# Kernel optimization log

Hardware: AMD Instinct MI355X
Metric: run time of the kernel (lower is better)

## Reference

```python
import jax, jax.numpy as jnp
import numpy as np

N = 50000   # nodes of ntype 'A'
E = 800000  # edges per metapath
M = 4       # metapaths (first-order, tail = 'A')
H = 4       # attn heads
C = 32      # out_channels = output_dim // attn_heads
IN = 256    # input_dim
D = H * C   # output_dim = 128
NEG_SLOPE = 0.2


def setup_inputs() -> dict:
    key = jax.random.key(0)
    ks = jax.random.split(key, 8)
    feats = jax.random.normal(ks[0], (N, IN), dtype=jnp.float32)
    edge_index = jax.random.randint(ks[1], (M, 2, E), 0, N, dtype=jnp.int32)
    W = jax.random.normal(ks[2], (IN, D), dtype=jnp.float32) * (2.0 / (IN + D)) ** 0.5
    b = jnp.zeros((D,), dtype=jnp.float32)
    attn = jax.random.normal(ks[3], (M, H, 2 * C), dtype=jnp.float32) * 0.1
    rel_attn_l = jax.random.normal(ks[4], (H, C), dtype=jnp.float32) * 0.1
    rel_attn_r = jax.random.normal(ks[5], (M + 1, H, C), dtype=jnp.float32) * 0.1
    rel_attn_bias = jnp.zeros((M + 1,), dtype=jnp.float32)
    return {"feats": feats, "edge_index": edge_index, "W": W, "b": b,
            "attn": attn, "rel_attn_l": rel_attn_l, "rel_attn_r": rel_attn_r,
            "rel_attn_bias": rel_attn_bias}


def _segment_softmax(logits, seg, num_segments):
    # logits: [E, H], seg: [E] target-node ids; softmax over incoming edges per node.
    seg_max = jax.ops.segment_max(logits, seg, num_segments=num_segments)  # [N, H]
    e = jnp.exp(logits - seg_max[seg])
    seg_sum = jax.ops.segment_sum(e, seg, num_segments=num_segments)       # [N, H]
    return e / (seg_sum[seg] + 1e-16)


def reference(feats, edge_index, W, b, attn, rel_attn_l, rel_attn_r, rel_attn_bias):
    # projection: per-ntype Linear + relu, reshape to heads
    h = jax.nn.relu(feats @ W + b).reshape(N, H, C)  # l_dict == r_dict == h

    # per-metapath GAT-style propagate (aggr='add')
    rels = []
    for m in range(M):
        src = edge_index[m, 0]
        dst = edge_index[m, 1]
        x_j = h[src]  # [E, H, C] source messages
        x_i = h[dst]  # [E, H, C] target queries
        # alpha = (cat([x_i, x_j], -1) * attn[m]).sum(-1), LeakyReLU(0.2)
        logits = jnp.einsum('ehc,hc->eh', x_i, attn[m, :, :C]) \
               + jnp.einsum('ehc,hc->eh', x_j, attn[m, :, C:])
        logits = jax.nn.leaky_relu(logits, NEG_SLOPE)
        alpha = _segment_softmax(logits, dst, N)                 # [E, H]
        out = jax.ops.segment_sum(x_j * alpha[..., None], dst, num_segments=N)  # [N, H, C]
        rels.append(out)
    rels.append(h)  # last relation slot = self (embedding[:, -1] = l_dict[ntype])
    emb = jnp.stack(rels, axis=1)  # [N, M+1, H, C]

    # beta relation-attention weights
    beta_l = jax.nn.relu(h * rel_attn_l)                          # [N, H, C]
    beta_r = jax.nn.relu(emb * rel_attn_r)                        # [N, M+1, H, C]
    beta = jnp.einsum('nhc,nrhc->nrh', beta_l, beta_r) + rel_attn_bias[None, :, None]
    beta = jax.nn.softmax(beta, axis=1)                           # over relations

    emb = (emb * beta[..., None]).sum(axis=1).reshape(N, D)
    return jax.nn.relu(emb)
```

## Files before the change

kernel.cpp:

```cpp
#include <hip/hip_runtime.h>
#include <math.h>

#define kN 50000
#define kE 800000
#define kM 4
#define kH 4
#define kC 32
#define kIN 256
#define kD 128

typedef __attribute__((ext_vector_type(8))) short bf16x8;
typedef __attribute__((ext_vector_type(4))) float f32x4;

__device__ __forceinline__ unsigned int f2bf_pack(float a, float b) {
    unsigned ua = __float_as_uint(a);
    ua += 0x7fffu + ((ua >> 16) & 1u);
    unsigned ub = __float_as_uint(b);
    ub += 0x7fffu + ((ub >> 16) & 1u);
    return (ua >> 16) | (ub & 0xffff0000u);
}
__device__ __forceinline__ unsigned short f2bf(float x) {
    unsigned u = __float_as_uint(x);
    u += 0x7fffu + ((u >> 16) & 1u);
    return (unsigned short)(u >> 16);
}

#define NBK 98
#define BCAP 10240
#define MW (NBK * BCAP)
#define PAB ((kE + 4095) / 4096)

__global__ void k_wcast(const float* __restrict__ W, unsigned short* __restrict__ Wt16) {
    const int col = blockIdx.x;
    const int k = threadIdx.x;
    Wt16[(size_t)col * kIN + k] = f2bf(W[(size_t)k * kD + col]);
}

#define GEMMB ((kN + 127) / 128)
__global__ __launch_bounds__(256) void k_gemmbucket(const float* __restrict__ feats,
                                                    const unsigned short* __restrict__ Wt16,
                                                    const float* __restrict__ b,
                                                    const float* __restrict__ attn,
                                                    unsigned short* __restrict__ h16,
                                                    float* __restrict__ sl,
                                                    float* __restrict__ sr,
                                                    const int* __restrict__ ei,
                                                    int* __restrict__ bcur,
                                                    unsigned int* __restrict__ pairs) {
    __shared__ __align__(16) unsigned char smem[64 * 130 * 2];
    __shared__ int hist[NBK], h2[NBK], base_s[NBK];
    const int t = threadIdx.x;

    if (blockIdx.x >= GEMMB) {
        const int bi = blockIdx.x - GEMMB;
        const int m = bi / PAB;
        const int chunk = bi - m * PAB;
        const int e0 = chunk * 4096;
        for (int j = t; j < NBK; j += 256) { hist[j] = 0; h2[j] = 0; }
        __syncthreads();
        int src[16], dst[16];
#pragma unroll
        for (int i = 0; i < 16; i++) {
            const int e = e0 + i * 256 + t;
            const int eok = (e < kE) ? e : 0;
            src[i] = ei[(size_t)m * 2 * kE + eok];
            dst[i] = (e < kE) ? ei[(size_t)m * 2 * kE + kE + eok] : -1;
        }
#pragma unroll
        for (int i = 0; i < 16; i++)
            if (dst[i] >= 0) atomicAdd(&hist[dst[i] >> 9], 1);
        __syncthreads();
        for (int j = t; j < NBK; j += 256)
            base_s[j] = atomicAdd(&bcur[m * NBK + j], hist[j]);
        __syncthreads();
#pragma unroll
        for (int i = 0; i < 16; i++) {
            if (dst[i] >= 0) {
                const int bk = dst[i] >> 9;
                const int slot = base_s[bk] + atomicAdd(&h2[bk], 1);
                pairs[(size_t)m * MW + (size_t)bk * BCAP + slot] =
                    ((unsigned int)(dst[i] & 511) << 16) | (unsigned int)src[i];
            }
        }
        return;
    }

    unsigned short* fr16 = reinterpret_cast<unsigned short*>(smem);
    typedef unsigned short hrow_t[130];
    hrow_t* hlds = reinterpret_cast<hrow_t*>(smem);

    const int lane = t & 63;
    const int wave = t >> 6;
    const int q = lane >> 4;
    const int m16 = lane & 15;
    const int wrow = (wave >> 1) * 64;
    const int wcol = (wave & 1) * 64;
    const int rowbase = blockIdx.x * 128;

    f32x4 acc[4][4];
#pragma unroll
    for (int i = 0; i < 4; i++)
#pragma unroll
        for (int j = 0; j < 4; j++) acc[i][j] = (f32x4){0.f, 0.f, 0.f, 0.f};

    const int srow = t >> 3;
    const int sk4 = t & 7;

    for (int kc = 0; kc < kIN; kc += 32) {
        __syncthreads();
#pragma unroll
        for (int it = 0; it < 4; it++) {
            const int row = srow + it * 32;
            const int rg = rowbase + row;
            float4 v = make_float4(0.f, 0.f, 0.f, 0.f);
            if (rg < kN)
                v = *reinterpret_cast<const float4*>(feats + (size_t)rg * kIN + kc + sk4 * 4);
            uint2 p;
            p.x = f2bf_pack(v.x, v.y);
            p.y = f2bf_pack(v.z, v.w);
            *reinterpret_cast<uint2*>(&fr16[row * 32 + sk4 * 4]) = p;
        }
        __syncthreads();

        bf16x8 afr[4], bfr[4];
#pragma unroll
        for (int ri = 0; ri < 4; ri++)
            afr[ri] = *reinterpret_cast<const bf16x8*>(
                &fr16[(wrow + ri * 16 + m16) * 32 + q * 8]);
#pragma unroll
        for (int ci = 0; ci < 4; ci++)
            bfr[ci] = *reinterpret_cast<const bf16x8*>(
                Wt16 + (size_t)(wcol + ci * 16 + m16) * kIN + kc + q * 8);
#pragma unroll
        for (int ri = 0; ri < 4; ri++)
#pragma unroll
            for (int ci = 0; ci < 4; ci++)
                acc[ri][ci] = __builtin_amdgcn_mfma_f32_16x16x32_bf16(
                    afr[ri], bfr[ci], acc[ri][ci], 0, 0, 0);
    }

    float bcol[4];
#pragma unroll
    for (int ci = 0; ci < 4; ci++) bcol[ci] = b[wcol + ci * 16 + m16];

#pragma unroll
    for (int ri = 0; ri < 4; ri++) {
#pragma unroll
        for (int reg = 0; reg < 4; reg++) {
            const int row = wrow + ri * 16 + q * 4 + reg;
            const int rg = rowbase + row;
            if (rg < kN) {
#pragma unroll
                for (int ci = 0; ci < 4; ci++) {
                    const int col = wcol + ci * 16 + m16;
                    const float v = fmaxf(acc[ri][ci][reg] + bcol[ci], 0.f);
                    h16[(size_t)rg * kD + col] = f2bf(v);
                }
            }
        }
    }
    __syncthreads();

    const unsigned int* hl32 = reinterpret_cast<const unsigned int*>(smem);
#pragma unroll
    for (int half = 0; half < 2; half++) {
        if ((wrow >> 6) == half) {
#pragma unroll
            for (int ri = 0; ri < 4; ri++)
#pragma unroll
                for (int reg = 0; reg < 4; reg++) {
                    const int row = (wrow & 63) + ri * 16 + q * 4 + reg;
#pragma unroll
                    for (int ci = 0; ci < 4; ci++) {
                        const int col = wcol + ci * 16 + m16;
                        const float v = fmaxf(acc[ri][ci][reg] + bcol[ci], 0.f);
                        hlds[row][col] = f2bf(v);
                    }
                }
        }
        __syncthreads();
        {
            const int hh = t & 3;
            const int nl = t >> 2;
            const int n = rowbase + half * 64 + nl;
            if (n < kN) {
                unsigned int u[16];
#pragma unroll
                for (int k = 0; k < 16; k++) u[k] = hl32[nl * 65 + hh * 16 + k];
                float f0[16], f1[16];
#pragma unroll
                for (int k = 0; k < 16; k++) {
                    f0[k] = __uint_as_float(u[k] << 16);
                    f1[k] = __uint_as_float(u[k] & 0xffff0000u);
                }
#pragma unroll
                for (int m = 0; m < kM; m++) {
                    const float2* al = reinterpret_cast<const float2*>(attn + (m * kH + hh) * 2 * kC);
                    const float2* ar = al + 16;
                    float s0 = 0.f, s1 = 0.f;
#pragma unroll
                    for (int k = 0; k < 16; k++) {
                        const float2 a = al[k], r = ar[k];
                        s0 += f0[k] * a.x + f1[k] * a.y;
                        s1 += f0[k] * r.x + f1[k] * r.y;
                    }
                    sl[((size_t)m * kN + n) * kH + hh] = s0;
                    sr[((size_t)m * kN + n) * kH + hh] = s1;
                }
            }
        }
        __syncthreads();
    }
}

#define SORTB (kM * NBK)
__global__ __launch_bounds__(256) void k_sort(const unsigned int* __restrict__ pairs,
                                              const int* __restrict__ bcur,
                                              int* __restrict__ offs,
                                              int* __restrict__ cnta,
                                              unsigned short* __restrict__ srcsort) {
    __shared__ int hist[512], pref[512], h2[512], wt[4];
    const int t = threadIdx.x;
    const int m = blockIdx.x / NBK;
    const int bk = blockIdx.x - m * NBK;
    const int bs = bk << 9;
    const int base = bk * BCAP;
    const int n = bcur[m * NBK + bk];
    const unsigned int* __restrict__ pb = pairs + (size_t)m * MW + base;
    unsigned short* __restrict__ ss = srcsort + (size_t)m * MW + base;

    hist[t] = 0; hist[t + 256] = 0; h2[t] = 0; h2[t + 256] = 0;
    __syncthreads();

    unsigned int v[40];
#pragma unroll
    for (int j = 0; j < 40; j++) {
        const int idx = j * 256 + t;
        v[j] = (idx < n) ? pb[idx] : 0xffffffffu;
    }
#pragma unroll
    for (int j = 0; j < 40; j++)
        if (v[j] != 0xffffffffu) atomicAdd(&hist[v[j] >> 16], 1);
    __syncthreads();

    const int lane = t & 63, wid = t >> 6;
    const int j0 = 2 * t, j1 = 2 * t + 1;
    const int h0 = hist[j0], h1 = hist[j1];
    const int s = h0 + h1;
    int incl = s;
#pragma unroll
    for (int d = 1; d < 64; d <<= 1) {
        const int x = __shfl_up(incl, d);
        if (lane >= d) incl += x;
    }
    if (lane == 63) wt[wid] = incl;
    __syncthreads();
    int woff = 0;
#pragma unroll
    for (int i = 0; i < 4; i++)
        if (i < wid) woff += wt[i];
    const int excl = woff + incl - s;
    pref[j0] = excl;
    pref[j1] = excl + h0;
    const int d0 = bs + j0, d1 = bs + j1;
    if (d0 < kN) { offs[m * kN + d0] = base + excl;       cnta[m * kN + d0] = h0; }
    if (d1 < kN) { offs[m * kN + d1] = base + excl + h0;  cnta[m * kN + d1] = h1; }
    __syncthreads();

#pragma unroll
    for (int j = 0; j < 40; j++) {
        if (v[j] != 0xffffffffu) {
            const int dl = (int)(v[j] >> 16);
            const int pos = pref[dl] + atomicAdd(&h2[dl], 1);
            ss[pos] = (unsigned short)(v[j] & 0xffffu);
        }
    }
    if (t < 64 && n + t < BCAP) ss[n + t] = 0;
}

#define CH 16

#define AGG_BODY(GN)                                                            \
    {                                                                           \
        int sj[GN];                                                             \
        _Pragma("unroll")                                                       \
        for (int j = 0; j < GN; j++) {                                          \
            const int id = __builtin_amdgcn_readlane(my0, j);                   \
            sj[j] = (j < nb) ? id : dst;                                        \
        }                                                                       \
        unsigned int u[GN];                                                     \
        _Pragma("unroll")                                                       \
        for (int j = 0; j < GN; j++)                                            \
            u[j] = *reinterpret_cast<const unsigned int*>(                      \
                hb + (((size_t)(unsigned int)sj[j] << 8) + ebyte));             \
        float x = sl_h + srv;                                                   \
        x = x > 0.f ? x : 0.2f * x;                         \
        const float w = (c + jj < cnt) ? __expf(x) : 0.f;                       \
        sum += w;                                                               \
        swts[m][l] = w;                                                         \
        __builtin_amdgcn_wave_barrier();                                        \
        const float4 w0 = *reinterpret_cast<const float4*>(&swts[m][hh * 16]);  \
        const float4 w1 = *reinterpret_cast<const float4*>(&swts[m][hh*16+4]);  \
        const float4 w2 = *reinterpret_cast<const float4*>(&swts[m][hh*16+8]);  \
        const float4 w3 = *reinterpret_cast<const float4*>(&swts[m][hh*16+12]); \
        __builtin_amdgcn_wave_barrier();                                        \
        my0 = my1;                                                              \
        my1 = sbase[c + 2 * CH + jj];                                           \
        srv = *reinterpret_cast<const float*>(                                  \
            srb + (((unsigned int)my0 << 4) + hbyte));                          \
        const float wj[16] = {w0.x, w0.y, w0.z, w0.w, w1.x, w1.y, w1.z, w1.w,   \
                              w2.x, w2.y, w2.z, w2.w, w3.x, w3.y, w3.z, w3.w};  \
        _Pragma("unroll")                                                       \
        for (int j = 0; j < GN; j++) {                                          \
            a0 += wj[j] * __uint_as_float(u[j] << 16);                          \
            a1 += wj[j] * __uint_as_float(u[j] & 0xffff0000u);                  \
        }                                                                       \
    }

__global__ __launch_bounds__(256) void k_agg(const unsigned short* __restrict__ h16,
                                             const float* __restrict__ sl,
                                             const float* __restrict__ sr,
                                             const int* __restrict__ offs,
                                             const int* __restrict__ cnta,
                                             const unsigned short* __restrict__ srcsort,
                                             const float* __restrict__ ral,
                                             const float* __restrict__ rar,
                                             const float* __restrict__ rbias,
                                             float* __restrict__ out) {
    const int dst = blockIdx.x;
    const int t = threadIdx.x;
    const int m = t >> 6;
    const int l = t & 63;
    const int hh = l >> 4;
    const int jj = l & 15;
    const int e0 = l * 2;

    __shared__ float smres[kM][kD];
    __shared__ float swts[kM][64];

    const int beg = offs[m * kN + dst];
    const int cnt = cnta[m * kN + dst];
    const float sl_h = sl[((size_t)m * kN + dst) * kH + hh];
    const unsigned short* __restrict__ sbase = srcsort + (size_t)m * MW + beg;
    const char* __restrict__ hb = (const char*)h16;
    const char* __restrict__ srb = (const char*)(sr + (size_t)m * kN * kH);
    const unsigned int ebyte = (unsigned int)(e0 << 1);
    const unsigned int hbyte = (unsigned int)(hh << 2);

    float sum = 0.f, a0 = 0.f, a1 = 0.f;

    int my0 = sbase[jj];
    int my1 = sbase[CH + jj];
    float srv = *reinterpret_cast<const float*>(
        srb + (((unsigned int)my0 << 4) + hbyte));

    for (int c = 0; c < cnt; c += CH) {
        const int nb = cnt - c;
        if (nb >= 9) AGG_BODY(16) else AGG_BODY(8)
    }

    sum += __shfl_xor(sum, 1);
    sum += __shfl_xor(sum, 2);
    sum += __shfl_xor(sum, 4);
    sum += __shfl_xor(sum, 8);
    const float inv = 1.0f / (sum + 1e-16f);
    smres[m][e0] = a0 * inv;
    smres[m][e0 + 1] = a1 * inv;
    __syncthreads();

    if (m == 0) {
        const unsigned int ud = *reinterpret_cast<const unsigned int*>(
            hb + (((unsigned int)dst << 8) + ebyte));
        const float hd0 = __uint_as_float(ud << 16);
        const float hd1 = __uint_as_float(ud & 0xffff0000u);
        const float bl0 = fmaxf(hd0 * ral[e0], 0.f);
        const float bl1 = fmaxf(hd1 * ral[e0 + 1], 0.f);
        float emb0[5], emb1[5], beta[5];
#pragma unroll
        for (int r = 0; r < 5; r++) {
            const float x0 = (r < 4) ? smres[r][e0] : hd0;
            const float x1 = (r < 4) ? smres[r][e0 + 1] : hd1;
            emb0[r] = x0;
            emb1[r] = x1;
            const float br0 = fmaxf(x0 * rar[r * kD + e0], 0.f);
            const float br1 = fmaxf(x1 * rar[r * kD + e0 + 1], 0.f);
            float p = bl0 * br0 + bl1 * br1;
            p += __shfl_xor(p, 1);
            p += __shfl_xor(p, 2);
            p += __shfl_xor(p, 4);
            p += __shfl_xor(p, 8);
            beta[r] = p + rbias[r];
        }
        float mx = beta[0];
#pragma unroll
        for (int r = 1; r < 5; r++) mx = fmaxf(mx, beta[r]);
        float s = 0.f, wgt[5];
#pragma unroll
        for (int r = 0; r < 5; r++) { wgt[r] = __expf(beta[r] - mx); s += wgt[r]; }
        const float invb = 1.f / s;
        float o0 = 0.f, o1 = 0.f;
#pragma unroll
        for (int r = 0; r < 5; r++) { o0 += emb0[r] * wgt[r]; o1 += emb1[r] * wgt[r]; }
        out[(size_t)dst * kD + e0] = fmaxf(o0 * invb, 0.f);
        out[(size_t)dst * kD + e0 + 1] = fmaxf(o1 * invb, 0.f);
    }
}

extern "C" void kernel_launch(void* const* d_in, const int* in_sizes, int n_in,
                              void* d_out, int out_size, void* d_ws, size_t ws_size,
                              hipStream_t stream) {
    const float* feats = (const float*)d_in[0];
    const int* ei      = (const int*)d_in[1];
    const float* W     = (const float*)d_in[2];
    const float* b     = (const float*)d_in[3];
    const float* attn  = (const float*)d_in[4];
    const float* ral   = (const float*)d_in[5];
    const float* rar   = (const float*)d_in[6];
    const float* rbias = (const float*)d_in[7];
    float* out = (float*)d_out;

    char* ws = (char*)d_ws;
    size_t off = 0;
    auto alloc = [&](size_t bytes) -> void* {
        void* p = ws + off;
        off = (off + bytes + 255) & ~(size_t)255;
        return p;
    };
    unsigned short* h16 = (unsigned short*)alloc(sizeof(short) * (size_t)kN * kD);
    unsigned short* Wt16= (unsigned short*)alloc(sizeof(short) * (size_t)kD * kIN);
    float* sl   = (float*)alloc(sizeof(float) * (size_t)kM * kN * kH);
    float* sr   = (float*)alloc(sizeof(float) * (size_t)kM * kN * kH);
    int* cnta   = (int*)alloc(sizeof(int) * (size_t)kM * kN);
    int* offs   = (int*)alloc(sizeof(int) * (size_t)kM * kN);
    int* bcur   = (int*)alloc(sizeof(int) * (kM * NBK + 64));
    unsigned short* srcsort =
        (unsigned short*)alloc(sizeof(short) * ((size_t)kM * MW + 64));
    unsigned int* pairs = (unsigned int*)alloc(sizeof(int) * (size_t)kM * MW);

    hipMemsetAsync(bcur, 0, sizeof(int) * (kM * NBK + 64), stream);
    k_wcast<<<kD, kIN, 0, stream>>>(W, Wt16);
    k_gemmbucket<<<GEMMB + kM * PAB, 256, 0, stream>>>(feats, Wt16, b, attn,
                                                       h16, sl, sr, ei, bcur, pairs);
    k_sort<<<SORTB, 256, 0, stream>>>(pairs, bcur, offs, cnta, srcsort);
    k_agg<<<kN, 256, 0, stream>>>(h16, sl, sr, offs, cnta, srcsort,
                                  ral, rar, rbias, out);
}
```

Baseline: 341.4 us.

## Split h and attention scores per head and map heads to XCDs in aggregation

Stores the projected features and the attention score arrays head-major, so each head's slice is a contiguous 3.2 MB region. The aggregation kernel now launches one block per (node, head), and the block index is decoded so that each pair of XCDs handles a single head. This is meant to keep each XCD's L2 working set inside one head's slice and cut cross-XCD cache misses on the random gathers. In exchange it launches four times as many blocks, each doing less work, adds shuffle-based reductions, and repeats the offset and count loads once per head.

```diff
diff --git a/kernel.cpp b/kernel.cpp
--- a/kernel.cpp
+++ b/kernel.cpp
@@ -41,9 +41,9 @@
                                                     const unsigned short* __restrict__ Wt16,
                                                     const float* __restrict__ b,
                                                     const float* __restrict__ attn,
-                                                    unsigned short* __restrict__ h16,
-                                                    float* __restrict__ sl,
-                                                    float* __restrict__ sr,
+                                                    unsigned short* __restrict__ h16t,
+                                                    float* __restrict__ slt,
+                                                    float* __restrict__ srt,
                                                     const int* __restrict__ ei,
                                                     int* __restrict__ bcur,
                                                     unsigned int* __restrict__ pairs) {
@@ -153,8 +153,9 @@
 #pragma unroll
                 for (int ci = 0; ci < 4; ci++) {
                     const int col = wcol + ci * 16 + m16;
+                    const int hd = col >> 5, ch = col & 31;
                     const float v = fmaxf(acc[ri][ci][reg] + bcol[ci], 0.f);
-                    h16[(size_t)rg * kD + col] = f2bf(v);
+                    h16t[((size_t)hd * kN + rg) * kC + ch] = f2bf(v);
                 }
             }
         }
@@ -180,8 +181,8 @@
         }
         __syncthreads();
         {
-            const int hh = t & 3;
-            const int nl = t >> 2;
+            const int hh = t >> 6;
+            const int nl = t & 63;
             const int n = rowbase + half * 64 + nl;
             if (n < kN) {
                 unsigned int u[16];
@@ -204,8 +205,8 @@
                         s0 += f0[k] * a.x + f1[k] * a.y;
                         s1 += f0[k] * r.x + f1[k] * r.y;
                     }
-                    sl[((size_t)m * kN + n) * kH + hh] = s0;
-                    sr[((size_t)m * kN + n) * kH + hh] = s1;
+                    slt[((size_t)hh * kM + m) * kN + n] = s0;
+                    srt[((size_t)hh * kM + m) * kN + n] = s1;
                 }
             }
         }
@@ -278,48 +279,10 @@
     if (t < 64 && n + t < BCAP) ss[n + t] = 0;
 }
 
-#define CH 16
-
-#define AGG_BODY(GN)                                                            \
-    {                                                                           \
-        int sj[GN];                                                             \
-        _Pragma("unroll")                                                       \
-        for (int j = 0; j < GN; j++) {                                          \
-            const int id = __builtin_amdgcn_readlane(my0, j);                   \
-            sj[j] = (j < nb) ? id : dst;                                        \
-        }                                                                       \
-        unsigned int u[GN];                                                     \
-        _Pragma("unroll")                                                       \
-        for (int j = 0; j < GN; j++)                                            \
-            u[j] = *reinterpret_cast<const unsigned int*>(                      \
-                hb + (((size_t)(unsigned int)sj[j] << 8) + ebyte));             \
-        float x = sl_h + srv;                                                   \
-        x = x > 0.f ? x : 0.2f * x;                         \
-        const float w = (c + jj < cnt) ? __expf(x) : 0.f;                       \
-        sum += w;                                                               \
-        swts[m][l] = w;                                                         \
-        __builtin_amdgcn_wave_barrier();                                        \
-        const float4 w0 = *reinterpret_cast<const float4*>(&swts[m][hh * 16]);  \
-        const float4 w1 = *reinterpret_cast<const float4*>(&swts[m][hh*16+4]);  \
-        const float4 w2 = *reinterpret_cast<const float4*>(&swts[m][hh*16+8]);  \
-        const float4 w3 = *reinterpret_cast<const float4*>(&swts[m][hh*16+12]); \
-        __builtin_amdgcn_wave_barrier();                                        \
-        my0 = my1;                                                              \
-        my1 = sbase[c + 2 * CH + jj];                                           \
-        srv = *reinterpret_cast<const float*>(                                  \
-            srb + (((unsigned int)my0 << 4) + hbyte));                          \
-        const float wj[16] = {w0.x, w0.y, w0.z, w0.w, w1.x, w1.y, w1.z, w1.w,   \
-                              w2.x, w2.y, w2.z, w2.w, w3.x, w3.y, w3.z, w3.w};  \
-        _Pragma("unroll")                                                       \
-        for (int j = 0; j < GN; j++) {                                          \
-            a0 += wj[j] * __uint_as_float(u[j] << 16);                          \
-            a1 += wj[j] * __uint_as_float(u[j] & 0xffff0000u);                  \
-        }                                                                       \
-    }
-
-__global__ __launch_bounds__(256) void k_agg(const unsigned short* __restrict__ h16,
-                                             const float* __restrict__ sl,
-                                             const float* __restrict__ sr,
+#define CH2 16
+__global__ __launch_bounds__(256) void k_agg(const unsigned short* __restrict__ h16t,
+                                             const float* __restrict__ slt,
+                                             const float* __restrict__ srt,
                                              const int* __restrict__ offs,
                                              const int* __restrict__ cnta,
                                              const unsigned short* __restrict__ srcsort,
@@ -327,63 +290,73 @@
                                              const float* __restrict__ rar,
                                              const float* __restrict__ rbias,
                                              float* __restrict__ out) {
-    const int dst = blockIdx.x;
+    const int i = blockIdx.x;
+    const int xcd = i & 7;
+    const int hh = xcd >> 1;
+    const int dst = ((i >> 3) << 1) | (xcd & 1);
     const int t = threadIdx.x;
     const int m = t >> 6;
     const int l = t & 63;
-    const int hh = l >> 4;
-    const int jj = l & 15;
-    const int e0 = l * 2;
-
-    __shared__ float smres[kM][kD];
-    __shared__ float swts[kM][64];
-
-    const int beg = offs[m * kN + dst];
-    const int cnt = cnta[m * kN + dst];
-    const float sl_h = sl[((size_t)m * kN + dst) * kH + hh];
+    const int cp = l & 15;
+    const int eg = l >> 4;
+
+    __shared__ float smres[kM][16][2];
+
+    const int beg = __builtin_nontemporal_load(&offs[m * kN + dst]);
+    const int cnt = __builtin_nontemporal_load(&cnta[m * kN + dst]);
+    const float sl_h = __builtin_nontemporal_load(&slt[((size_t)hh * kM + m) * kN + dst]);
     const unsigned short* __restrict__ sbase = srcsort + (size_t)m * MW + beg;
-    const char* __restrict__ hb = (const char*)h16;
-    const char* __restrict__ srb = (const char*)(sr + (size_t)m * kN * kH);
-    const unsigned int ebyte = (unsigned int)(e0 << 1);
-    const unsigned int hbyte = (unsigned int)(hh << 2);
+    const char* __restrict__ hb = (const char*)(h16t + (size_t)hh * kN * kC);
+    const float* __restrict__ srb = srt + ((size_t)hh * kM + m) * kN;
+    const unsigned int cbyte = (unsigned int)(cp << 2);
 
     float sum = 0.f, a0 = 0.f, a1 = 0.f;
 
-    int my0 = sbase[jj];
-    int my1 = sbase[CH + jj];
-    float srv = *reinterpret_cast<const float*>(
-        srb + (((unsigned int)my0 << 4) + hbyte));
-
-    for (int c = 0; c < cnt; c += CH) {
-        const int nb = cnt - c;
-        if (nb >= 9) AGG_BODY(16) else AGG_BODY(8)
-    }
-
-    sum += __shfl_xor(sum, 1);
-    sum += __shfl_xor(sum, 2);
-    sum += __shfl_xor(sum, 4);
-    sum += __shfl_xor(sum, 8);
+    for (int c = 0; c < cnt; c += CH2) {
+        const int idv = (int)__builtin_nontemporal_load(&sbase[c + cp]);
+        const float srv = srb[idv];
+        float x = sl_h + srv;
+        x = x > 0.f ? x : 0.2f * x;
+        const float w = (c + cp < cnt) ? __expf(x) : 0.f;
+        float ws = w;
+        ws += __shfl_xor(ws, 1); ws += __shfl_xor(ws, 2);
+        ws += __shfl_xor(ws, 4); ws += __shfl_xor(ws, 8);
+        sum += ws;
+#pragma unroll
+        for (int k = 0; k < 4; k++) {
+            const int e = eg * 4 + k;
+            const int id = __shfl(idv, e);
+            const float wk = __shfl(w, e);
+            const int row = (c + e < cnt) ? id : dst;
+            const unsigned int u = *reinterpret_cast<const unsigned int*>(
+                hb + (((unsigned int)row << 6) + cbyte));
+            a0 += wk * __uint_as_float(u << 16);
+            a1 += wk * __uint_as_float(u & 0xffff0000u);
+        }
+    }
+    a0 += __shfl_xor(a0, 16); a0 += __shfl_xor(a0, 32);
+    a1 += __shfl_xor(a1, 16); a1 += __shfl_xor(a1, 32);
     const float inv = 1.0f / (sum + 1e-16f);
-    smres[m][e0] = a0 * inv;
-    smres[m][e0 + 1] = a1 * inv;
-    __syncthreads();
-
-    if (m == 0) {
+    if (l < 16) { smres[m][cp][0] = a0 * inv; smres[m][cp][1] = a1 * inv; }
+    __syncthreads();
+
+    if (m == 0 && l < 16) {
         const unsigned int ud = *reinterpret_cast<const unsigned int*>(
-            hb + (((unsigned int)dst << 8) + ebyte));
+            hb + (((unsigned int)dst << 6) + cbyte));
         const float hd0 = __uint_as_float(ud << 16);
         const float hd1 = __uint_as_float(ud & 0xffff0000u);
-        const float bl0 = fmaxf(hd0 * ral[e0], 0.f);
-        const float bl1 = fmaxf(hd1 * ral[e0 + 1], 0.f);
+        const int ch = hh * kC + cp * 2;
+        const float bl0 = fmaxf(hd0 * ral[ch], 0.f);
+        const float bl1 = fmaxf(hd1 * ral[ch + 1], 0.f);
         float emb0[5], emb1[5], beta[5];
 #pragma unroll
         for (int r = 0; r < 5; r++) {
-            const float x0 = (r < 4) ? smres[r][e0] : hd0;
-            const float x1 = (r < 4) ? smres[r][e0 + 1] : hd1;
+            const float x0 = (r < 4) ? smres[r][cp][0] : hd0;
+            const float x1 = (r < 4) ? smres[r][cp][1] : hd1;
             emb0[r] = x0;
             emb1[r] = x1;
-            const float br0 = fmaxf(x0 * rar[r * kD + e0], 0.f);
-            const float br1 = fmaxf(x1 * rar[r * kD + e0 + 1], 0.f);
+            const float br0 = fmaxf(x0 * rar[r * kD + ch], 0.f);
+            const float br1 = fmaxf(x1 * rar[r * kD + ch + 1], 0.f);
             float p = bl0 * br0 + bl1 * br1;
             p += __shfl_xor(p, 1);
             p += __shfl_xor(p, 2);
@@ -401,8 +374,8 @@
         float o0 = 0.f, o1 = 0.f;
 #pragma unroll
         for (int r = 0; r < 5; r++) { o0 += emb0[r] * wgt[r]; o1 += emb1[r] * wgt[r]; }
-        out[(size_t)dst * kD + e0] = fmaxf(o0 * invb, 0.f);
-        out[(size_t)dst * kD + e0 + 1] = fmaxf(o1 * invb, 0.f);
+        __builtin_nontemporal_store(fmaxf(o0 * invb, 0.f), &out[(size_t)dst * kD + ch]);
+        __builtin_nontemporal_store(fmaxf(o1 * invb, 0.f), &out[(size_t)dst * kD + ch + 1]);
     }
 }
 
@@ -442,6 +415,6 @@
     k_gemmbucket<<<GEMMB + kM * PAB, 256, 0, stream>>>(feats, Wt16, b, attn,
                                                        h16, sl, sr, ei, bcur, pairs);
     k_sort<<<SORTB, 256, 0, stream>>>(pairs, bcur, offs, cnta, srcsort);
-    k_agg<<<kN, 256, 0, stream>>>(h16, sl, sr, offs, cnta, srcsort,
-                                  ral, rar, rbias, out);
-}
+    k_agg<<<kN * kH, 256, 0, stream>>>(h16, sl, sr, offs, cnta, srcsort,
+                                       ral, rar, rbias, out);
+}
```

Result: slower. 577.1 us (+69.0%).
